# Optimization experiments

Measured on AMD Instinct MI355X. Metric: run time of the kernel, lower is better.

The kernel has to match this reference:

```python
import jax, jax.numpy as jnp
import numpy as np

B, S, H, F, E, TOPK = 2, 1024, 1024, 2816, 8, 2

def setup_inputs() -> dict:
    key = jax.random.key(0)
    k1, k2, k3, k4 = jax.random.split(key, 4)
    return {
        "hidden_states": jax.random.normal(k1, (B, S, H), dtype=jnp.float32),
        "gate_w": jax.random.normal(k2, (E, H), dtype=jnp.float32) * 0.02,  # gate 1x1 conv == [E,H] matrix
        "w1": jax.random.normal(k3, (E, F, H), dtype=jnp.float32) * 0.02,   # per-expert up-proj
        "w2": jax.random.normal(k4, (E, H, F), dtype=jnp.float32) * 0.02,   # per-expert down-proj
        "top_k": TOPK,
    }

def reference(hidden_states, gate_w, w1, w2, top_k):
    b, s, h = hidden_states.shape
    e = gate_w.shape[0]
    x = hidden_states.reshape(-1, h)                       # [N, H]
    n = x.shape[0]
    # Router: 1x1 conv gate == linear, softmax, top-k, renormalize
    logits = x @ gate_w.T                                  # [N, E]
    probs = jax.nn.softmax(logits, axis=-1)
    topw, topi = jax.lax.top_k(probs, top_k)               # [N, k]
    topw = topw / jnp.sum(topw, axis=-1, keepdims=True)
    # Per-(token, expert) combine weight; zero for non-selected experts.
    # Equivalent to torch.where(topk_indices == e, topk_weights, 0).sum(-1).
    comb = jnp.zeros((n, e), dtype=x.dtype).at[jnp.arange(n)[:, None], topi].add(topw)  # [N, E]
    # Expert MLPs (1x1 convs == GEMMs): up -> SiLU -> down, weighted combine.
    up = jnp.einsum('nh,efh->nef', x, w1)                  # [N, E, F]
    act = jax.nn.silu(up)
    out = jnp.einsum('nef,ehf->neh', act, w2)              # [N, E, H]
    y = jnp.einsum('ne,neh->nh', comb, out)                # weighted combine
    return y.reshape(b, s, h)
```

## Files before the change

### kernel.cpp

```cpp
#include <hip/hip_runtime.h>
#include <hip/hip_bf16.h>
#include <stdint.h>

#define N_TOK 2048
#define H_DIM 1024
#define F_DIM 2816
#define N_EXP 8

#define BK 64
#define LDA 72

typedef __attribute__((ext_vector_type(8))) short bf16x8;
typedef __attribute__((ext_vector_type(4))) float f32x4;

static __device__ __forceinline__ unsigned short f2bf(float f) {
    union { float f; unsigned u; } v; v.f = f;
    unsigned r = v.u + 0x7fffu + ((v.u >> 16) & 1u);
    return (unsigned short)(r >> 16);
}

__global__ __launch_bounds__(256) void router_kernel(
    const float* __restrict__ x, const float* __restrict__ gate_w,
    int* __restrict__ counts, int* __restrict__ row_token, float* __restrict__ row_weight,
    int* __restrict__ slot_e, int* __restrict__ slot_pos)
{
    __shared__ float gsm[N_EXP * H_DIM];
    for (int i = threadIdx.x; i < N_EXP * H_DIM; i += 256) gsm[i] = gate_w[i];
    __syncthreads();

    const int wave = threadIdx.x >> 6;
    const int lane = threadIdx.x & 63;
    const int n = blockIdx.x * 4 + wave;
    if (n >= N_TOK) return;

    float xv[16];
#pragma unroll
    for (int i = 0; i < 16; i++) xv[i] = x[(size_t)n * H_DIM + lane + 64 * i];

    float logit[N_EXP];
#pragma unroll
    for (int e = 0; e < N_EXP; e++) {
        float p = 0.f;
#pragma unroll
        for (int i = 0; i < 16; i++) p += xv[i] * gsm[e * H_DIM + lane + 64 * i];
#pragma unroll
        for (int s = 32; s > 0; s >>= 1) p += __shfl_xor(p, s, 64);
        logit[e] = p;
    }

    if (lane == 0) {
        int e0 = 0; float l0 = logit[0];
#pragma unroll
        for (int e = 1; e < N_EXP; e++) if (logit[e] > l0) { l0 = logit[e]; e0 = e; }
        int e1 = -1; float l1 = -3.4e38f;
#pragma unroll
        for (int e = 0; e < N_EXP; e++) if (e != e0 && logit[e] > l1) { l1 = logit[e]; e1 = e; }
        float w0 = 1.f / (1.f + __expf(l1 - l0));
        float w1 = 1.f - w0;
        int p0 = atomicAdd(&counts[e0], 1);
        int p1 = atomicAdd(&counts[e1], 1);
        row_token[e0 * N_TOK + p0] = n;  row_weight[e0 * N_TOK + p0] = w0;
        row_token[e1 * N_TOK + p1] = n;  row_weight[e1 * N_TOK + p1] = w1;
        slot_e[n * 2 + 0] = e0;  slot_pos[n * 2 + 0] = p0;
        slot_e[n * 2 + 1] = e1;  slot_pos[n * 2 + 1] = p1;
    }
}

__global__ void scan_kernel(const int* __restrict__ counts, int* __restrict__ offsets)
{
    if (threadIdx.x == 0 && blockIdx.x == 0) {
        int acc = 0;
        for (int e = 0; e < N_EXP; e++) { offsets[e] = acc; acc += counts[e]; }
    }
}

__global__ __launch_bounds__(256) void up_gemm_kernel(
    const float* __restrict__ x, const float* __restrict__ w1,
    const int* __restrict__ counts, const int* __restrict__ offsets,
    const int* __restrict__ row_token,
    unsigned short* __restrict__ act)
{
    const int e = blockIdx.z;
    const int cnt = counts[e];
    const int mTile = blockIdx.y;
    if (mTile * 128 >= cnt) return;
    const int fTile = blockIdx.x;
    const int off = offsets[e];

    __shared__ __align__(16) unsigned short As[128 * LDA];
    __shared__ __align__(16) unsigned short Bs[128 * LDA];

    const int tid = threadIdx.x;
    const int lane = tid & 63;
    const int wave = tid >> 6;
    const int wm = (wave >> 1) * 64, wn = (wave & 1) * 64;

    int tokens[8];
#pragma unroll
    for (int j = 0; j < 8; j++) {
        int i = tid + 256 * j;
        int row = i >> 4;
        int pos = mTile * 128 + row;
        tokens[j] = row_token[e * N_TOK + min(pos, cnt - 1)];
    }

    f32x4 acc[4][4];
#pragma unroll
    for (int i = 0; i < 4; i++)
#pragma unroll
        for (int j = 0; j < 4; j++) acc[i][j] = (f32x4)(0.f);

    const float* wbase = w1 + (size_t)e * F_DIM * H_DIM + (size_t)(fTile * 128) * H_DIM;

    for (int kt = 0; kt < H_DIM / BK; kt++) {
        const int k0 = kt * BK;
#pragma unroll
        for (int j = 0; j < 8; j++) {
            int i = tid + 256 * j;
            int row = i >> 4, c = i & 15;
            const float4 v = *(const float4*)(x + (size_t)tokens[j] * H_DIM + k0 + c * 4);
            ushort4 b; b.x = f2bf(v.x); b.y = f2bf(v.y); b.z = f2bf(v.z); b.w = f2bf(v.w);
            *(ushort4*)(As + row * LDA + c * 4) = b;
        }
#pragma unroll
        for (int j = 0; j < 8; j++) {
            int i = tid + 256 * j;
            int row = i >> 4, c = i & 15;
            const float4 v = *(const float4*)(wbase + (size_t)row * H_DIM + k0 + c * 4);
            ushort4 b; b.x = f2bf(v.x); b.y = f2bf(v.y); b.z = f2bf(v.z); b.w = f2bf(v.w);
            *(ushort4*)(Bs + row * LDA + c * 4) = b;
        }
        __syncthreads();
#pragma unroll
        for (int ks = 0; ks < BK / 32; ks++) {
            const int kloc = ks * 32 + (lane >> 4) * 8;
            bf16x8 af[4], bfr[4];
#pragma unroll
            for (int i = 0; i < 4; i++)
                af[i] = *(const bf16x8*)(As + (wm + i * 16 + (lane & 15)) * LDA + kloc);
#pragma unroll
            for (int i = 0; i < 4; i++)
                bfr[i] = *(const bf16x8*)(Bs + (wn + i * 16 + (lane & 15)) * LDA + kloc);
#pragma unroll
            for (int i = 0; i < 4; i++)
#pragma unroll
                for (int j = 0; j < 4; j++)
                    acc[i][j] = __builtin_amdgcn_mfma_f32_16x16x32_bf16(af[i], bfr[j], acc[i][j], 0, 0, 0);
        }
        __syncthreads();
    }

#pragma unroll
    for (int i = 0; i < 4; i++) {
        const int mrow = wm + i * 16 + ((lane >> 4) << 2);
#pragma unroll
        for (int r = 0; r < 4; r++) {
            const int m = mTile * 128 + mrow + r;
            if (m < cnt) {
#pragma unroll
                for (int j = 0; j < 4; j++) {
                    float v = acc[i][j][r];
                    float s = v / (1.f + __expf(-v));
                    int col = fTile * 128 + wn + j * 16 + (lane & 15);
                    act[(size_t)(off + m) * F_DIM + col] = f2bf(s);
                }
            }
        }
    }
}

__global__ __launch_bounds__(256) void down_gemm_kernel(
    const unsigned short* __restrict__ act, const float* __restrict__ w2,
    const int* __restrict__ counts, const int* __restrict__ offsets,
    const float* __restrict__ row_weight,
    float* __restrict__ out_slot)
{
    const int e = blockIdx.z;
    const int cnt = counts[e];
    const int mTile = blockIdx.y;
    if (mTile * 128 >= cnt) return;
    const int hTile = blockIdx.x;
    const int off = offsets[e];

    __shared__ __align__(16) unsigned short As[128 * LDA];
    __shared__ __align__(16) unsigned short Bs[128 * LDA];

    const int tid = threadIdx.x;
    const int lane = tid & 63;
    const int wave = tid >> 6;
    const int wm = (wave >> 1) * 64, wn = (wave & 1) * 64;

    int rowsg[4];
#pragma unroll
    for (int j = 0; j < 4; j++) {
        int i = tid + 256 * j;
        int row = i >> 3;
        rowsg[j] = off + min(mTile * 128 + row, cnt - 1);
    }

    f32x4 acc[4][4];
#pragma unroll
    for (int i = 0; i < 4; i++)
#pragma unroll
        for (int j = 0; j < 4; j++) acc[i][j] = (f32x4)(0.f);

    const float* wbase = w2 + (size_t)e * H_DIM * F_DIM + (size_t)(hTile * 128) * F_DIM;

    for (int kt = 0; kt < F_DIM / BK; kt++) {
        const int k0 = kt * BK;
#pragma unroll
        for (int j = 0; j < 4; j++) {
            int i = tid + 256 * j;
            int row = i >> 3, c = i & 7;
            const uint4 v = *(const uint4*)(act + (size_t)rowsg[j] * F_DIM + k0 + c * 8);
            *(uint4*)(As + row * LDA + c * 8) = v;
        }
#pragma unroll
        for (int j = 0; j < 8; j++) {
            int i = tid + 256 * j;
            int row = i >> 4, c = i & 15;
            const float4 v = *(const float4*)(wbase + (size_t)row * F_DIM + k0 + c * 4);
            ushort4 b; b.x = f2bf(v.x); b.y = f2bf(v.y); b.z = f2bf(v.z); b.w = f2bf(v.w);
            *(ushort4*)(Bs + row * LDA + c * 4) = b;
        }
        __syncthreads();
#pragma unroll
        for (int ks = 0; ks < BK / 32; ks++) {
            const int kloc = ks * 32 + (lane >> 4) * 8;
            bf16x8 af[4], bfr[4];
#pragma unroll
            for (int i = 0; i < 4; i++)
                af[i] = *(const bf16x8*)(As + (wm + i * 16 + (lane & 15)) * LDA + kloc);
#pragma unroll
            for (int i = 0; i < 4; i++)
                bfr[i] = *(const bf16x8*)(Bs + (wn + i * 16 + (lane & 15)) * LDA + kloc);
#pragma unroll
            for (int i = 0; i < 4; i++)
#pragma unroll
                for (int j = 0; j < 4; j++)
                    acc[i][j] = __builtin_amdgcn_mfma_f32_16x16x32_bf16(af[i], bfr[j], acc[i][j], 0, 0, 0);
        }
        __syncthreads();
    }

#pragma unroll
    for (int i = 0; i < 4; i++) {
        const int mrow = wm + i * 16 + ((lane >> 4) << 2);
#pragma unroll
        for (int r = 0; r < 4; r++) {
            const int m = mTile * 128 + mrow + r;
            if (m < cnt) {
                const float w = row_weight[e * N_TOK + m];
#pragma unroll
                for (int j = 0; j < 4; j++) {
                    int col = hTile * 128 + wn + j * 16 + (lane & 15);
                    out_slot[(size_t)(off + m) * H_DIM + col] = w * acc[i][j][r];
                }
            }
        }
    }
}

__global__ __launch_bounds__(256) void combine_kernel(
    const float* __restrict__ out_slot, const int* __restrict__ offsets,
    const int* __restrict__ slot_e, const int* __restrict__ slot_pos,
    float* __restrict__ out)
{
    const int n = blockIdx.x;
    const int r0 = offsets[slot_e[n * 2 + 0]] + slot_pos[n * 2 + 0];
    const int r1 = offsets[slot_e[n * 2 + 1]] + slot_pos[n * 2 + 1];
    const int t = threadIdx.x;
    const float4 a = *(const float4*)(out_slot + (size_t)r0 * H_DIM + t * 4);
    const float4 b = *(const float4*)(out_slot + (size_t)r1 * H_DIM + t * 4);
    float4 c; c.x = a.x + b.x; c.y = a.y + b.y; c.z = a.z + b.z; c.w = a.w + b.w;
    *(float4*)(out + (size_t)n * H_DIM + t * 4) = c;
}

extern "C" void kernel_launch(void* const* d_in, const int* in_sizes, int n_in,
                              void* d_out, int out_size, void* d_ws, size_t ws_size,
                              hipStream_t stream) {
    const float* x      = (const float*)d_in[0];
    const float* gate_w = (const float*)d_in[1];
    const float* w1     = (const float*)d_in[2];
    const float* w2     = (const float*)d_in[3];
    float* out = (float*)d_out;

    char* ws = (char*)d_ws;
    size_t o = 0;
    auto alloc = [&](size_t bytes) -> void* {
        void* p = ws + o;
        o = (o + bytes + 255) & ~(size_t)255;
        return p;
    };
    int*   counts     = (int*)  alloc(N_EXP * sizeof(int));
    int*   offsets    = (int*)  alloc(N_EXP * sizeof(int));
    int*   row_token  = (int*)  alloc((size_t)N_EXP * N_TOK * sizeof(int));
    float* row_weight = (float*)alloc((size_t)N_EXP * N_TOK * sizeof(float));
    int*   slot_e     = (int*)  alloc((size_t)N_TOK * 2 * sizeof(int));
    int*   slot_pos   = (int*)  alloc((size_t)N_TOK * 2 * sizeof(int));
    unsigned short* act = (unsigned short*)alloc((size_t)N_TOK * 2 * F_DIM * sizeof(unsigned short));
    float* out_slot   = (float*)alloc((size_t)N_TOK * 2 * H_DIM * sizeof(float));

    hipMemsetAsync(counts, 0, N_EXP * sizeof(int), stream);

    router_kernel<<<N_TOK / 4, 256, 0, stream>>>(x, gate_w, counts, row_token, row_weight, slot_e, slot_pos);
    scan_kernel<<<1, 64, 0, stream>>>(counts, offsets);
    up_gemm_kernel<<<dim3(F_DIM / 128, N_TOK / 128, N_EXP), 256, 0, stream>>>(
        x, w1, counts, offsets, row_token, act);
    down_gemm_kernel<<<dim3(H_DIM / 128, N_TOK / 128, N_EXP), 256, 0, stream>>>(
        act, w2, counts, offsets, row_weight, out_slot);
    combine_kernel<<<N_TOK, 256, 0, stream>>>(out_slot, offsets, slot_e, slot_pos, out);
}
```

Baseline: 402.3 us.

## Pre-convert x to bf16, register-prefetch GEMM tiles, split-K down-proj with atomic combine

The router now also writes a bf16 copy of x, so the up-projection gathers half as many bytes and skips per-tile conversion. Both GEMMs prefetch the next K tile into registers while the current tile is being computed. The down-projection is split into two K halves and atomically adds weighted results straight into the zeroed output, which removes the out_slot buffer and the combine kernel. The cost is extra memsets, float atomics with nondeterministic summation order, and more register pressure.

```diff
diff --git a/kernel.cpp b/kernel.cpp
--- a/kernel.cpp
+++ b/kernel.cpp
@@ -22,7 +22,7 @@
 __global__ __launch_bounds__(256) void router_kernel(
     const float* __restrict__ x, const float* __restrict__ gate_w,
     int* __restrict__ counts, int* __restrict__ row_token, float* __restrict__ row_weight,
-    int* __restrict__ slot_e, int* __restrict__ slot_pos)
+    unsigned short* __restrict__ xb)
 {
     __shared__ float gsm[N_EXP * H_DIM];
     for (int i = threadIdx.x; i < N_EXP * H_DIM; i += 256) gsm[i] = gate_w[i];
@@ -31,11 +31,13 @@
     const int wave = threadIdx.x >> 6;
     const int lane = threadIdx.x & 63;
     const int n = blockIdx.x * 4 + wave;
-    if (n >= N_TOK) return;
 
     float xv[16];
 #pragma unroll
     for (int i = 0; i < 16; i++) xv[i] = x[(size_t)n * H_DIM + lane + 64 * i];
+
+#pragma unroll
+    for (int i = 0; i < 16; i++) xb[(size_t)n * H_DIM + lane + 64 * i] = f2bf(xv[i]);
 
     float logit[N_EXP];
 #pragma unroll
@@ -61,8 +63,6 @@
         int p1 = atomicAdd(&counts[e1], 1);
         row_token[e0 * N_TOK + p0] = n;  row_weight[e0 * N_TOK + p0] = w0;
         row_token[e1 * N_TOK + p1] = n;  row_weight[e1 * N_TOK + p1] = w1;
-        slot_e[n * 2 + 0] = e0;  slot_pos[n * 2 + 0] = p0;
-        slot_e[n * 2 + 1] = e1;  slot_pos[n * 2 + 1] = p1;
     }
 }
 
@@ -75,7 +75,7 @@
 }
 
 __global__ __launch_bounds__(256) void up_gemm_kernel(
-    const float* __restrict__ x, const float* __restrict__ w1,
+    const unsigned short* __restrict__ xb, const float* __restrict__ w1,
     const int* __restrict__ counts, const int* __restrict__ offsets,
     const int* __restrict__ row_token,
     unsigned short* __restrict__ act)
@@ -95,13 +95,11 @@
     const int wave = tid >> 6;
     const int wm = (wave >> 1) * 64, wn = (wave & 1) * 64;
 
-    int tokens[8];
-#pragma unroll
-    for (int j = 0; j < 8; j++) {
-        int i = tid + 256 * j;
-        int row = i >> 4;
-        int pos = mTile * 128 + row;
-        tokens[j] = row_token[e * N_TOK + min(pos, cnt - 1)];
+    int tokens[4];
+#pragma unroll
+    for (int j = 0; j < 4; j++) {
+        int row = (tid + 256 * j) >> 3;
+        tokens[j] = row_token[e * N_TOK + min(mTile * 128 + row, cnt - 1)];
     }
 
     f32x4 acc[4][4];
@@ -112,25 +110,43 @@
 
     const float* wbase = w1 + (size_t)e * F_DIM * H_DIM + (size_t)(fTile * 128) * H_DIM;
 
-    for (int kt = 0; kt < H_DIM / BK; kt++) {
-        const int k0 = kt * BK;
+    uint4 ra[4];
+    float4 rb[8];
+    auto loadA = [&](int kt) {
+#pragma unroll
+        for (int j = 0; j < 4; j++) {
+            int i = tid + 256 * j; int c = i & 7;
+            ra[j] = *(const uint4*)(xb + (size_t)tokens[j] * H_DIM + kt * BK + c * 8);
+        }
+    };
+    auto loadB = [&](int kt) {
 #pragma unroll
         for (int j = 0; j < 8; j++) {
-            int i = tid + 256 * j;
-            int row = i >> 4, c = i & 15;
-            const float4 v = *(const float4*)(x + (size_t)tokens[j] * H_DIM + k0 + c * 4);
-            ushort4 b; b.x = f2bf(v.x); b.y = f2bf(v.y); b.z = f2bf(v.z); b.w = f2bf(v.w);
-            *(ushort4*)(As + row * LDA + c * 4) = b;
+            int i = tid + 256 * j; int row = i >> 4, c = i & 15;
+            rb[j] = *(const float4*)(wbase + (size_t)row * H_DIM + kt * BK + c * 4);
+        }
+    };
+    auto stage = [&] {
+#pragma unroll
+        for (int j = 0; j < 4; j++) {
+            int i = tid + 256 * j; int row = i >> 3, c = i & 7;
+            *(uint4*)(As + row * LDA + c * 8) = ra[j];
         }
 #pragma unroll
         for (int j = 0; j < 8; j++) {
-            int i = tid + 256 * j;
-            int row = i >> 4, c = i & 15;
-            const float4 v = *(const float4*)(wbase + (size_t)row * H_DIM + k0 + c * 4);
+            int i = tid + 256 * j; int row = i >> 4, c = i & 15;
+            float4 v = rb[j];
             ushort4 b; b.x = f2bf(v.x); b.y = f2bf(v.y); b.z = f2bf(v.z); b.w = f2bf(v.w);
             *(ushort4*)(Bs + row * LDA + c * 4) = b;
         }
+    };
+
+    const int NKT = H_DIM / BK;
+    loadA(0); loadB(0);
+    for (int kt = 0; kt < NKT; kt++) {
+        stage();
         __syncthreads();
+        if (kt + 1 < NKT) { loadA(kt + 1); loadB(kt + 1); }
 #pragma unroll
         for (int ks = 0; ks < BK / 32; ks++) {
             const int kloc = ks * 32 + (lane >> 4) * 8;
@@ -172,10 +188,11 @@
 __global__ __launch_bounds__(256) void down_gemm_kernel(
     const unsigned short* __restrict__ act, const float* __restrict__ w2,
     const int* __restrict__ counts, const int* __restrict__ offsets,
-    const float* __restrict__ row_weight,
-    float* __restrict__ out_slot)
+    const int* __restrict__ row_token, const float* __restrict__ row_weight,
+    float* __restrict__ out)
 {
-    const int e = blockIdx.z;
+    const int e = blockIdx.z >> 1;
+    const int ksplit = blockIdx.z & 1;
     const int cnt = counts[e];
     const int mTile = blockIdx.y;
     if (mTile * 128 >= cnt) return;
@@ -193,8 +210,7 @@
     int rowsg[4];
 #pragma unroll
     for (int j = 0; j < 4; j++) {
-        int i = tid + 256 * j;
-        int row = i >> 3;
+        int row = (tid + 256 * j) >> 3;
         rowsg[j] = off + min(mTile * 128 + row, cnt - 1);
     }
 
@@ -206,24 +222,44 @@
 
     const float* wbase = w2 + (size_t)e * H_DIM * F_DIM + (size_t)(hTile * 128) * F_DIM;
 
-    for (int kt = 0; kt < F_DIM / BK; kt++) {
-        const int k0 = kt * BK;
+    uint4 ra[4];
+    float4 rb[8];
+    auto loadA = [&](int kt) {
 #pragma unroll
         for (int j = 0; j < 4; j++) {
-            int i = tid + 256 * j;
-            int row = i >> 3, c = i & 7;
-            const uint4 v = *(const uint4*)(act + (size_t)rowsg[j] * F_DIM + k0 + c * 8);
-            *(uint4*)(As + row * LDA + c * 8) = v;
-        }
+            int i = tid + 256 * j; int c = i & 7;
+            ra[j] = *(const uint4*)(act + (size_t)rowsg[j] * F_DIM + kt * BK + c * 8);
+        }
+    };
+    auto loadB = [&](int kt) {
 #pragma unroll
         for (int j = 0; j < 8; j++) {
-            int i = tid + 256 * j;
-            int row = i >> 4, c = i & 15;
-            const float4 v = *(const float4*)(wbase + (size_t)row * F_DIM + k0 + c * 4);
+            int i = tid + 256 * j; int row = i >> 4, c = i & 15;
+            rb[j] = *(const float4*)(wbase + (size_t)row * F_DIM + kt * BK + c * 4);
+        }
+    };
+    auto stage = [&] {
+#pragma unroll
+        for (int j = 0; j < 4; j++) {
+            int i = tid + 256 * j; int row = i >> 3, c = i & 7;
+            *(uint4*)(As + row * LDA + c * 8) = ra[j];
+        }
+#pragma unroll
+        for (int j = 0; j < 8; j++) {
+            int i = tid + 256 * j; int row = i >> 4, c = i & 15;
+            float4 v = rb[j];
             ushort4 b; b.x = f2bf(v.x); b.y = f2bf(v.y); b.z = f2bf(v.z); b.w = f2bf(v.w);
             *(ushort4*)(Bs + row * LDA + c * 4) = b;
         }
+    };
+
+    const int KT_PER = (F_DIM / BK) / 2;
+    const int kt0 = ksplit * KT_PER;
+    loadA(kt0); loadB(kt0);
+    for (int kt = kt0; kt < kt0 + KT_PER; kt++) {
+        stage();
         __syncthreads();
+        if (kt + 1 < kt0 + KT_PER) { loadA(kt + 1); loadB(kt + 1); }
 #pragma unroll
         for (int ks = 0; ks < BK / 32; ks++) {
             const int kloc = ks * 32 + (lane >> 4) * 8;
@@ -250,30 +286,16 @@
         for (int r = 0; r < 4; r++) {
             const int m = mTile * 128 + mrow + r;
             if (m < cnt) {
+                const int tok = row_token[e * N_TOK + m];
                 const float w = row_weight[e * N_TOK + m];
 #pragma unroll
                 for (int j = 0; j < 4; j++) {
                     int col = hTile * 128 + wn + j * 16 + (lane & 15);
-                    out_slot[(size_t)(off + m) * H_DIM + col] = w * acc[i][j][r];
+                    atomicAdd(out + (size_t)tok * H_DIM + col, w * acc[i][j][r]);
                 }
             }
         }
     }
-}
-
-__global__ __launch_bounds__(256) void combine_kernel(
-    const float* __restrict__ out_slot, const int* __restrict__ offsets,
-    const int* __restrict__ slot_e, const int* __restrict__ slot_pos,
-    float* __restrict__ out)
-{
-    const int n = blockIdx.x;
-    const int r0 = offsets[slot_e[n * 2 + 0]] + slot_pos[n * 2 + 0];
-    const int r1 = offsets[slot_e[n * 2 + 1]] + slot_pos[n * 2 + 1];
-    const int t = threadIdx.x;
-    const float4 a = *(const float4*)(out_slot + (size_t)r0 * H_DIM + t * 4);
-    const float4 b = *(const float4*)(out_slot + (size_t)r1 * H_DIM + t * 4);
-    float4 c; c.x = a.x + b.x; c.y = a.y + b.y; c.z = a.z + b.z; c.w = a.w + b.w;
-    *(float4*)(out + (size_t)n * H_DIM + t * 4) = c;
 }
 
 extern "C" void kernel_launch(void* const* d_in, const int* in_sizes, int n_in,
@@ -296,18 +318,16 @@
     int*   offsets    = (int*)  alloc(N_EXP * sizeof(int));
     int*   row_token  = (int*)  alloc((size_t)N_EXP * N_TOK * sizeof(int));
     float* row_weight = (float*)alloc((size_t)N_EXP * N_TOK * sizeof(float));
-    int*   slot_e     = (int*)  alloc((size_t)N_TOK * 2 * sizeof(int));
-    int*   slot_pos   = (int*)  alloc((size_t)N_TOK * 2 * sizeof(int));
+    unsigned short* xb  = (unsigned short*)alloc((size_t)N_TOK * H_DIM * sizeof(unsigned short));
     unsigned short* act = (unsigned short*)alloc((size_t)N_TOK * 2 * F_DIM * sizeof(unsigned short));
-    float* out_slot   = (float*)alloc((size_t)N_TOK * 2 * H_DIM * sizeof(float));
 
     hipMemsetAsync(counts, 0, N_EXP * sizeof(int), stream);
-
-    router_kernel<<<N_TOK / 4, 256, 0, stream>>>(x, gate_w, counts, row_token, row_weight, slot_e, slot_pos);
+    hipMemsetAsync(out, 0, (size_t)out_size * sizeof(float), stream);
+
+    router_kernel<<<N_TOK / 4, 256, 0, stream>>>(x, gate_w, counts, row_token, row_weight, xb);
     scan_kernel<<<1, 64, 0, stream>>>(counts, offsets);
     up_gemm_kernel<<<dim3(F_DIM / 128, N_TOK / 128, N_EXP), 256, 0, stream>>>(
-        x, w1, counts, offsets, row_token, act);
-    down_gemm_kernel<<<dim3(H_DIM / 128, N_TOK / 128, N_EXP), 256, 0, stream>>>(
-        act, w2, counts, offsets, row_weight, out_slot);
-    combine_kernel<<<N_TOK, 256, 0, stream>>>(out_slot, offsets, slot_e, slot_pos, out);
-}
+        xb, w1, counts, offsets, row_token, act);
+    down_gemm_kernel<<<dim3(H_DIM / 128, N_TOK / 128, N_EXP * 2), 256, 0, stream>>>(
+        act, w2, counts, offsets, row_token, row_weight, out);
+}
```

After: 481.4 us. 1.2x slower.
